# Kernel tuning notes

Hardware: AMD Instinct MI355X
Metric: run time of the kernel (lower is better)

Reference implementation:

```python
import jax, jax.numpy as jnp
import numpy as np

V, E, H, B, TE, TD = 32000, 256, 256, 32, 128, 64


def _gru_cell(x, h, Wi, Wh, bi, bh):
    # PyTorch GRU gate order: r, z, n
    gi = x @ Wi.T + bi            # [B, 3H]
    gh = h @ Wh.T + bh            # [B, 3H]
    i_r, i_z, i_n = jnp.split(gi, 3, axis=-1)
    h_r, h_z, h_n = jnp.split(gh, 3, axis=-1)
    r = jax.nn.sigmoid(i_r + h_r)
    z = jax.nn.sigmoid(i_z + h_z)
    n = jnp.tanh(i_n + r * h_n)
    return (1.0 - z) * n + z * h


def _run_gru(x_seq, h0, Wi, Wh, bi, bh, reverse=False):
    # x_seq: [B, T, D] -> outputs [B, T, H]
    xs = jnp.swapaxes(x_seq, 0, 1)  # [T, B, D]
    def step(h, x_t):
        h = _gru_cell(x_t, h, Wi, Wh, bi, bh)
        return h, h
    _, ys = jax.lax.scan(step, h0, xs, reverse=reverse)
    return jnp.swapaxes(ys, 0, 1)


def setup_inputs() -> dict:
    key = jax.random.key(0)
    ks = jax.random.split(key, 22)
    k = 1.0 / np.sqrt(H)
    u = lambda kk, shape, a: jax.random.uniform(kk, shape, jnp.float32, -a, a)
    return {
        'enc_in': jax.random.randint(ks[0], (B, TE), 0, V),
        'dec_in': jax.random.randint(ks[1], (B, TD), 0, V),
        'embed_W': u(ks[2], (V, E), 0.1),
        'Wi_f': u(ks[3], (3 * H, E), k), 'Wh_f': u(ks[4], (3 * H, H), k),
        'bi_f': u(ks[5], (3 * H,), k), 'bh_f': u(ks[6], (3 * H,), k),
        'Wi_b': u(ks[7], (3 * H, E), k), 'Wh_b': u(ks[8], (3 * H, H), k),
        'bi_b': u(ks[9], (3 * H,), k), 'bh_b': u(ks[10], (3 * H,), k),
        'Wi_d': u(ks[11], (3 * H, E + 2 * H), k), 'Wh_d': u(ks[12], (3 * H, H), k),
        'bi_d': u(ks[13], (3 * H,), k), 'bh_d': u(ks[14], (3 * H,), k),
        'W1_w': u(ks[15], (H, 2 * H), 1.0 / np.sqrt(2 * H)), 'W1_b': u(ks[16], (H,), 1.0 / np.sqrt(2 * H)),
        'W2_w': u(ks[17], (2 * H, H), k), 'W2_b': u(ks[18], (2 * H,), k),
        'lin_w': u(ks[19], (V, H), 0.1), 'lin_b': jnp.zeros((V,), jnp.float32),
    }


def reference(enc_in, dec_in, embed_W, Wi_f, Wh_f, bi_f, bh_f, Wi_b, Wh_b, bi_b, bh_b,
              Wi_d, Wh_d, bi_d, bh_d, W1_w, W1_b, W2_w, W2_b, lin_w, lin_b):
    # ---- encoder (bidirectional GRU, 1 layer) ----
    enc_emb = embed_W[enc_in]                                   # [B, TE, E]
    h0 = jnp.zeros((B, H), enc_emb.dtype)
    out_f = _run_gru(enc_emb, h0, Wi_f, Wh_f, bi_f, bh_f)       # [B, TE, H]
    out_b = _run_gru(enc_emb, h0, Wi_b, Wh_b, bi_b, bh_b, reverse=True)
    encoded = jnp.concatenate([out_f, out_b], axis=-1)          # [B, TE, 2H]

    # last valid state per example: encoded[i, sizes[i]-1]
    sizes = (enc_in > 0).sum(axis=1)                            # [B]
    last_states = encoded[jnp.arange(B), sizes - 1]             # [B, 2H]

    # ---- decoder with Luong attention (teacher forcing) ----
    dec_emb = embed_W[dec_in]                                   # [B, TD, E]
    h_init = last_states @ W1_w.T + W1_b                        # [B, H]
    ctx_init = jnp.zeros((B, 2 * H), enc_emb.dtype)

    def dec_step(carry, x_t):
        h, ctx = carry
        inp = jnp.concatenate([ctx, x_t], axis=-1)              # [B, E+2H]
        h = _gru_cell(inp, h, Wi_d, Wh_d, bi_d, bh_d)           # [B, H]
        comp = h @ W2_w.T + W2_b                                # [B, 2H]
        scores = jax.nn.softmax(jnp.einsum('bte,be->bt', encoded, comp), axis=-1)
        ctx = jnp.einsum('bt,bte->be', scores, encoded)          # [B, 2H]
        return (h, ctx), h

    _, outs = jax.lax.scan(dec_step, (h_init, ctx_init), jnp.swapaxes(dec_emb, 0, 1))
    outs = jnp.swapaxes(outs, 0, 1)                             # [B, TD, H]
    logits = outs @ lin_w.T + lin_b                             # [B, TD, V]
    return logits
```

## Files before the change

kernel.cpp:

```cpp
#include <hip/hip_runtime.h>
#include <hip/hip_bf16.h>

#define Vv 32000
#define Ee 256
#define Hh 256
#define Bb 32
#define TEe 128
#define TDd 64

typedef __attribute__((ext_vector_type(4))) float f32x4;
typedef __attribute__((ext_vector_type(8))) short short8;
typedef __attribute__((ext_vector_type(2))) unsigned int uint2v;
typedef __attribute__((ext_vector_type(4))) unsigned int uint4v;

static __device__ __forceinline__ unsigned short f2bf(float f){
  unsigned u = __float_as_uint(f);
  u += 0x7fffu + ((u >> 16) & 1u);
  return (unsigned short)(u >> 16);
}
static __device__ __forceinline__ unsigned pack2(float a, float b){
  return ((unsigned)f2bf(b) << 16) | (unsigned)f2bf(a);
}
static __device__ __forceinline__ float dot8(uint4v u, const float* hh){
  float s = 0.f;
  #pragma unroll
  for (int i = 0; i < 4; ++i){
    unsigned w = u[i];
    s = fmaf(__uint_as_float(w << 16),        hh[2*i],   s);
    s = fmaf(__uint_as_float(w & 0xffff0000u), hh[2*i+1], s);
  }
  return s;
}
static __device__ __forceinline__ float sigmoidf_(float x){
  return 1.f / (1.f + __expf(-x));
}

__global__ void k_sizes(const int* __restrict__ enc_in, int* __restrict__ sizes){
  int b = threadIdx.x;
  if (b < Bb){
    int c = 0;
    for (int t = 0; t < TEe; ++t) c += (enc_in[b*TEe + t] > 0);
    sizes[b] = c;
  }
}

__global__ void k_gather(const int* __restrict__ tok, const float* __restrict__ embW,
                         float* __restrict__ out, int rows){
  int i = blockIdx.x * 256 + threadIdx.x;
  int r = i >> 8, c = i & 255;
  if (r < rows) out[i] = embW[(size_t)tok[r]*Ee + c];
}

__global__ void k_extract_bf16(const float* __restrict__ src, unsigned short* __restrict__ dst,
                               int n){
  int i = blockIdx.x * 256 + threadIdx.x;
  if (i < n) dst[i] = f2bf(src[i]);
}

__global__ void k_chunkw(const float* __restrict__ src, unsigned short* __restrict__ dst, int rows){
  int idx = blockIdx.x * 256 + threadIdx.x;
  if (idx < rows * 256){
    int i = idx & 7, r = (idx >> 3) % rows, kb = idx / (rows * 8);
    dst[idx] = f2bf(src[(size_t)r*256 + kb*8 + i]);
  }
}

__global__ void k_projchunk(const float* __restrict__ in, unsigned short* __restrict__ out){
  int idx = blockIdx.x * 256 + threadIdx.x;
  int i = idx & 7;
  int t1 = idx >> 3;
  int n = t1 % 768;
  int t2 = t1 / 768;
  int kb = t2 & 15, b = t2 >> 4;
  out[idx] = f2bf(in[(size_t)(b*TEe + kb*8 + i)*768 + n]);
}

template<bool A_BF16, bool B_BF16, bool B_KMAJOR, bool OUT_BF16>
__global__ __launch_bounds__(256) void k_gemm(
  const void* __restrict__ Av, const void* __restrict__ Bv,
  const float* __restrict__ bias, void* __restrict__ Cv,
  int M, int N, int K, int lda, int ldb, int ldc)
{
  __shared__ unsigned short lA[128*40];
  __shared__ unsigned short lB[128*40];
  const int tid  = threadIdx.x;
  const int lane = tid & 63;
  const int w = tid >> 6, wr = w >> 1, wc = w & 1;
  const int m0 = blockIdx.y * 128, n0 = blockIdx.x * 128;
  f32x4 acc[4][4];
  #pragma unroll
  for (int i = 0; i < 4; ++i)
    #pragma unroll
    for (int j = 0; j < 4; ++j) acc[i][j] = (f32x4){0.f,0.f,0.f,0.f};

  for (int k0 = 0; k0 < K; k0 += 32){
    if (A_BF16){
      const unsigned short* A = (const unsigned short*)Av;
      #pragma unroll
      for (int it = 0; it < 2; ++it){
        int idx = tid + it*256; int r = idx >> 2, q = idx & 3;
        *(uint4v*)&lA[r*40 + q*8] = *(const uint4v*)(A + (size_t)(m0+r)*lda + k0 + q*8);
      }
    } else {
      const float* A = (const float*)Av;
      #pragma unroll
      for (int it = 0; it < 4; ++it){
        int idx = tid + it*256; int r = idx >> 3, q = idx & 7;
        f32x4 v = *(const f32x4*)(A + (size_t)(m0+r)*lda + k0 + q*4);
        uint2v pk; pk[0] = pack2(v[0], v[1]); pk[1] = pack2(v[2], v[3]);
        *(uint2v*)&lA[r*40 + q*4] = pk;
      }
    }
    if (B_KMAJOR){
      const float* Bp = (const float*)Bv;
      #pragma unroll
      for (int it = 0; it < 4; ++it){
        int idx = tid + it*256; int kk = idx >> 5, nq = idx & 31;
        f32x4 v = *(const f32x4*)(Bp + (size_t)(k0+kk)*ldb + n0 + nq*4);
        #pragma unroll
        for (int s2 = 0; s2 < 4; ++s2) lB[(nq*4+s2)*40 + kk] = f2bf(v[s2]);
      }
    } else if (B_BF16){
      const unsigned short* Bp = (const unsigned short*)Bv;
      #pragma unroll
      for (int it = 0; it < 2; ++it){
        int idx = tid + it*256; int r = idx >> 2, q = idx & 3;
        *(uint4v*)&lB[r*40 + q*8] = *(const uint4v*)(Bp + (size_t)(n0+r)*ldb + k0 + q*8);
      }
    } else {
      const float* Bp = (const float*)Bv;
      #pragma unroll
      for (int it = 0; it < 4; ++it){
        int idx = tid + it*256; int r = idx >> 3, q = idx & 7;
        f32x4 v = *(const f32x4*)(Bp + (size_t)(n0+r)*ldb + k0 + q*4);
        uint2v pk; pk[0] = pack2(v[0], v[1]); pk[1] = pack2(v[2], v[3]);
        *(uint2v*)&lB[r*40 + q*4] = pk;
      }
    }
    __syncthreads();
    short8 av[4], bv[4];
    #pragma unroll
    for (int i = 0; i < 4; ++i)
      av[i] = *(const short8*)&lA[(wr*64 + i*16 + (lane&15))*40 + (lane>>4)*8];
    #pragma unroll
    for (int j = 0; j < 4; ++j)
      bv[j] = *(const short8*)&lB[(wc*64 + j*16 + (lane&15))*40 + (lane>>4)*8];
    #pragma unroll
    for (int i = 0; i < 4; ++i)
      #pragma unroll
      for (int j = 0; j < 4; ++j)
        acc[i][j] = __builtin_amdgcn_mfma_f32_16x16x32_bf16(av[i], bv[j], acc[i][j], 0, 0, 0);
    __syncthreads();
  }
  #pragma unroll
  for (int i = 0; i < 4; ++i){
    #pragma unroll
    for (int j = 0; j < 4; ++j){
      int col = n0 + wc*64 + j*16 + (lane & 15);
      float bb = bias ? bias[col] : 0.f;
      #pragma unroll
      for (int r = 0; r < 4; ++r){
        int row = m0 + wr*64 + i*16 + (lane>>4)*4 + r;
        float v = acc[i][j][r] + bb;
        if (OUT_BF16) ((unsigned short*)Cv)[(size_t)row*ldc + col] = f2bf(v);
        else          ((float*)Cv)[(size_t)row*ldc + col] = v;
      }
    }
  }
}

__global__ __launch_bounds__(1024) void k_encoder(
  const unsigned short* __restrict__ Whf, const unsigned short* __restrict__ Whb,
  const float* __restrict__ bhf, const float* __restrict__ bhb,
  const float* __restrict__ gif, const float* __restrict__ gib,
  float* __restrict__ encoded)
{
  extern __shared__ char smem[];
  unsigned short* lw = (unsigned short*)smem;
  float* hA   = (float*)(smem + 131072);
  float* hB   = (float*)(smem + 132096);
  float* parA = (float*)(smem + 133120);
  float* parB = (float*)(smem + 137216);
  const int dir = blockIdx.x & 1, b = blockIdx.x >> 1;
  const unsigned short* Wh = dir ? Whb : Whf;
  const float* bh = dir ? bhb : bhf;
  const float* gi = dir ? gib : gif;
  const int T = threadIdx.x;
  const int rl = T & 255, q4 = T >> 8;
  const int rrh = T & 511, hf = T >> 9;
  const unsigned short* wsrc = Wh + (size_t)(hf*16)*6144 + (size_t)(256 + rrh)*8;
  uint4v wb[8];
  #pragma unroll
  for (int d = 0; d < 8; ++d) wb[d] = *(const uint4v*)(wsrc + (size_t)d*6144);
  for (int cc = T; cc < 256*32; cc += 1024){
    int r = cc >> 5, q = cc & 31;
    *(uint4v*)&lw[(r*32 + (q ^ (r & 31)))*8] = *(const uint4v*)(Wh + (size_t)q*6144 + r*8);
  }
  float bh0 = 0.f, bh1 = 0.f, bh2 = 0.f;
  if (T < 256){ bh0 = bh[T]; bh1 = bh[T+256]; bh2 = bh[T+512]; hA[T] = 0.f; }
  __syncthreads();
  const float* hc = hA; float* hn = hB;
  for (int s = 0; s < TEe; ++s){
    const int t = dir ? (TEe-1-s) : s;
    float aL = 0.f;
    #pragma unroll
    for (int i = 0; i < 8; ++i){
      const int ck = q4*8 + i;
      float hr[8];
      *(f32x4*)&hr[0] = *(const f32x4*)&hc[ck*8];
      *(f32x4*)&hr[4] = *(const f32x4*)&hc[ck*8+4];
      aL += dot8(*(const uint4v*)&lw[(rl*32 + (ck ^ (rl & 31)))*8], hr);
    }
    parA[q4*256 + rl] = aL;
    float aR = 0.f;
    const float* hh = hc + hf*128;
    #pragma unroll
    for (int q = 0; q < 16; ++q){
      float hr[8];
      *(f32x4*)&hr[0] = *(const f32x4*)&hh[q*8];
      *(f32x4*)&hr[4] = *(const f32x4*)&hh[q*8+4];
      aR += dot8(wb[q & 7], hr);
      wb[q & 7] = *(const uint4v*)(wsrc + (size_t)((q < 8) ? (q + 8) : (q - 8))*6144);
    }
    parB[hf*512 + rrh] = aR;
    __syncthreads();
    if (T < 256){
      const int j = T;
      const float* grow = gi + (size_t)(b*TEe + t)*768;
      const float A0 = parA[j] + parA[256+j] + parA[512+j] + parA[768+j] + bh0;
      const float A1 = parB[j] + parB[512+j] + bh1;
      const float A2 = parB[256+j] + parB[768+j] + bh2;
      const float r = sigmoidf_(grow[j] + A0);
      const float z = sigmoidf_(grow[j+256] + A1);
      const float n = tanhf(grow[j+512] + r*A2);
      const float hnew = (1.f - z)*n + z*hc[j];
      hn[j] = hnew;
      encoded[(size_t)(b*TEe + t)*512 + dir*256 + j] = hnew;
    }
    __syncthreads();
    const float* tmp = hc; hc = hn; hn = (float*)tmp;
  }
}

__global__ void k_encb2(const float* __restrict__ encoded, const float* __restrict__ W2b,
                        float* __restrict__ encb2){
  int r = blockIdx.x, l = threadIdx.x;
  const float* e = encoded + (size_t)r*512;
  float s = 0.f;
  for (int k = l; k < 512; k += 64) s += e[k]*W2b[k];
  for (int off = 32; off; off >>= 1) s += __shfl_down(s, off);
  if (l == 0) encb2[r] = s;
}

__global__ void k_hinit(const float* __restrict__ encoded, const int* __restrict__ sizes,
                        const float* __restrict__ W1w, const float* __restrict__ W1b,
                        float* __restrict__ h0){
  int b = blockIdx.x, o = threadIdx.x;
  int idx = sizes[b] - 1;
  idx = idx < 0 ? 0 : (idx > TEe-1 ? TEe-1 : idx);
  const float* ls = encoded + (size_t)(b*TEe + idx)*512;
  const float* wv = W1w + (size_t)o*512;
  float s = W1b[o];
  for (int k = 0; k < 512; k += 4){
    f32x4 a = *(const f32x4*)(ls + k);
    f32x4 w4 = *(const f32x4*)(wv + k);
    s = fmaf(a[0],w4[0], fmaf(a[1],w4[1], fmaf(a[2],w4[2], fmaf(a[3],w4[3], s))));
  }
  h0[b*256 + o] = s;
}

#define DLR 128
__global__ __launch_bounds__(512, 1) void k_decoder(
  const unsigned short* __restrict__ Whd, const float* __restrict__ bhd,
  const float* __restrict__ gidx,
  const unsigned short* __restrict__ encw2,
  const float* __restrict__ encb2,
  const unsigned short* __restrict__ projt,
  const float* __restrict__ h0,
  unsigned short* __restrict__ outs_bf)
{
  extern __shared__ char smem[];
  unsigned short* le = (unsigned short*)smem;
  unsigned short* lw = (unsigned short*)(smem + 65536);
  float* h    = (float*)(smem + 131072);
  float* parL = (float*)(smem + 132096);
  float* parS1= (float*)(smem + 134144);
  float* parS2= (float*)(smem + 136192);
  float* gcs  = (float*)(smem + 138240);
  float* cpar = (float*)(smem + 140288);
  float* p    = (float*)(smem + 142336);
  float* ebl  = (float*)(smem + 142848);
  const int b = blockIdx.x, T = threadIdx.x;
  const unsigned short* ptc = projt + (size_t)b*98304;
  const unsigned short* wsrcM = Whd + (size_t)(DLR + T)*8;
  const int trow = 640 + (T >> 2), tq = (T & 3)*8;
  const unsigned short* wsrcT = Whd + (size_t)trow*8;
  const unsigned short* csrcM = ptc + (size_t)T*8;
  const int crow = 512 + (T >> 1), cq = (T & 1)*8;
  const unsigned short* csrcT = ptc + (size_t)crow*8;
  uint4v wb[8], wb2[2], cb[4], cb2[2];
  #pragma unroll
  for (int d = 0; d < 8; ++d) wb[d] = *(const uint4v*)(wsrcM + (size_t)d*6144);
  wb2[0] = *(const uint4v*)(wsrcT + (size_t)tq*6144);
  wb2[1] = *(const uint4v*)(wsrcT + (size_t)(tq+1)*6144);
  #pragma unroll
  for (int d = 0; d < 4; ++d) cb[d] = *(const uint4v*)(csrcM + (size_t)d*6144);
  cb2[0] = *(const uint4v*)(csrcT + (size_t)cq*6144);
  cb2[1] = *(const uint4v*)(csrcT + (size_t)(cq+1)*6144);
  for (int cc = T; cc < 128*32; cc += 512){
    int r = cc >> 5, q = cc & 31;
    *(uint4v*)&le[(r*32 + (q ^ (r & 31)))*8] =
        *(const uint4v*)(encw2 + ((size_t)(b*TEe + r) << 8) + (q << 3));
  }
  for (int cc = T; cc < DLR*32; cc += 512){
    int r = cc >> 5, q = cc & 31;
    *(uint4v*)&lw[(r*32 + (q ^ (r & 31)))*8] =
        *(const uint4v*)(Whd + (size_t)q*6144 + r*8);
  }
  for (int i = T; i < 256; i += 512) h[i] = h0[b*256 + i];
  gcs[T] = 0.f; cpar[T] = 0.f;
  if (T < TEe) ebl[T] = encb2[b*TEe + T];
  float bh0 = 0.f, bh1 = 0.f, bh2 = 0.f;
  if (T < 256){ bh0 = bhd[T]; bh1 = bhd[T+256]; bh2 = bhd[T+512]; }
  __syncthreads();
  float g0 = 0.f, g1 = 0.f, g2 = 0.f;
  if (T < 256){
    const float* grow = gidx + (size_t)(b*TDd)*768;
    g0 = grow[T]; g1 = grow[T+256]; g2 = grow[T+512];
  }
  #define DOTS_BODY                                                            \
  {                                                                            \
    { const int rL2 = T >> 2, qb = (T & 3)*8;                                  \
      const unsigned short* lwr = lw + rL2*256;                                \
      float a = 0.f;                                                           \
      _Pragma("unroll")                                                        \
      for (int i = 0; i < 8; ++i){                                             \
        const int q = qb + i;                                                  \
        float hr[8];                                                           \
        *(f32x4*)&hr[0] = *(const f32x4*)&h[q*8];                              \
        *(f32x4*)&hr[4] = *(const f32x4*)&h[q*8+4];                            \
        a += dot8(*(const uint4v*)(lwr + ((q ^ (rL2 & 31)) << 3)), hr);        \
      }                                                                        \
      parL[(T & 3)*128 + rL2] = a;                                             \
    }                                                                          \
    { float a = 0.f;                                                           \
      _Pragma("unroll")                                                        \
      for (int q = 0; q < 32; ++q){                                            \
        float hr[8];                                                           \
        *(f32x4*)&hr[0] = *(const f32x4*)&h[q*8];                              \
        *(f32x4*)&hr[4] = *(const f32x4*)&h[q*8+4];                            \
        a += dot8(wb[q & 7], hr);                                              \
        wb[q & 7] = *(const uint4v*)(wsrcM + (size_t)((q < 24) ? (q + 8) : (q - 24))*6144); \
      }                                                                        \
      parS1[T] = a;                                                            \
    }                                                                          \
    { float a = 0.f;                                                           \
      _Pragma("unroll")                                                        \
      for (int i = 0; i < 8; ++i){                                             \
        const int q = tq + i;                                                  \
        float hr[8];                                                           \
        *(f32x4*)&hr[0] = *(const f32x4*)&h[q*8];                              \
        *(f32x4*)&hr[4] = *(const f32x4*)&h[q*8+4];                            \
        a += dot8(wb2[i & 1], hr);                                             \
        wb2[i & 1] = *(const uint4v*)(wsrcT + (size_t)(tq + ((i < 6) ? (i + 2) : (i - 6)))*6144); \
      }                                                                        \
      parS2[(T & 3)*128 + (T >> 2)] = a;                                       \
    }                                                                          \
  }
  DOTS_BODY
  __syncthreads();
  for (int t = 0; t < TDd; ++t){
    if (T < 256){
      const int j = T;
      float A0, A2;
      if (j < 128){
        A0 = parL[j] + parL[128+j] + parL[256+j] + parL[384+j];
        A2 = parS1[384+j];
      } else {
        A0 = parS1[j-128];
        A2 = parS2[j-128] + parS2[j] + parS2[j+128] + parS2[j+256];
      }
      const float A1 = parS1[128+j];
      const float gcr = gcs[j];
      const float gcz = gcs[256+j];
      const float gcn = cpar[j] + cpar[256+j];
      const float r = sigmoidf_(g0 + gcr + A0 + bh0);
      const float z = sigmoidf_(g1 + gcz + A1 + bh1);
      const float n = tanhf(g2 + gcn + r*(A2 + bh2));
      const float hnew = (1.f - z)*n + z*h[j];
      h[j] = hnew;
      outs_bf[(size_t)(b*TDd + t)*256 + j] = f2bf(hnew);
    }
    if (t + 1 == TDd) break;
    __syncthreads();
    if (T < 256){
      const float* grow = gidx + (size_t)(b*TDd + t + 1)*768;
      g0 = grow[T]; g1 = grow[T+256]; g2 = grow[T+512];
    }
    DOTS_BODY
    {
      const int pos = T >> 2, kq = (T & 3)*8;
      const unsigned short* er = le + pos*256;
      float s = 0.f;
      #pragma unroll
      for (int i = 0; i < 8; ++i){
        const int q = kq + i;
        float hr[8];
        *(f32x4*)&hr[0] = *(const f32x4*)&h[q*8];
        *(f32x4*)&hr[4] = *(const f32x4*)&h[q*8+4];
        s += dot8(*(const uint4v*)(er + ((q ^ (pos & 31)) << 3)), hr);
      }
      s += __shfl_xor(s, 1);
      s += __shfl_xor(s, 2);
      if ((T & 3) == 0) p[pos] = s + ebl[pos];
    }
    __syncthreads();
    if (T < 64){
      float m = fmaxf(p[T], p[T+64]);
      for (int off = 32; off; off >>= 1) m = fmaxf(m, __shfl_xor(m, off));
      float e0 = __expf(p[T] - m), e1 = __expf(p[T+64] - m);
      float ss = e0 + e1;
      for (int off = 32; off; off >>= 1) ss += __shfl_xor(ss, off);
      float inv = 1.f / ss;
      p[T] = e0*inv; p[T+64] = e1*inv;
    }
    __syncthreads();
    {
      float c = 0.f;
      #pragma unroll
      for (int q = 0; q < 16; ++q){
        float pr[8];
        *(f32x4*)&pr[0] = *(const f32x4*)&p[q*8];
        *(f32x4*)&pr[4] = *(const f32x4*)&p[q*8+4];
        c += dot8(cb[q & 3], pr);
        cb[q & 3] = *(const uint4v*)(csrcM + (size_t)((q < 12) ? (q + 4) : (q - 12))*6144);
      }
      gcs[T] = c;
      float c2 = 0.f;
      #pragma unroll
      for (int i = 0; i < 8; ++i){
        const int q = cq + i;
        float pr[8];
        *(f32x4*)&pr[0] = *(const f32x4*)&p[q*8];
        *(f32x4*)&pr[4] = *(const f32x4*)&p[q*8+4];
        c2 += dot8(cb2[i & 1], pr);
        cb2[i & 1] = *(const uint4v*)(csrcT + (size_t)(cq + ((i < 6) ? (i + 2) : (i - 6)))*6144);
      }
      cpar[(T & 1)*256 + (T >> 1)] = c2;
    }
    __syncthreads();
  }
  #undef DOTS_BODY
}

extern "C" void kernel_launch(void* const* d_in, const int* in_sizes, int n_in,
                              void* d_out, int out_size, void* d_ws, size_t ws_size,
                              hipStream_t stream)
{
  (void)in_sizes; (void)n_in; (void)out_size;
  const int*   enc_in = (const int*)d_in[0];
  const int*   dec_in = (const int*)d_in[1];
  const float* embW   = (const float*)d_in[2];
  const float* Wi_f   = (const float*)d_in[3];
  const float* Wh_f   = (const float*)d_in[4];
  const float* bi_f   = (const float*)d_in[5];
  const float* bh_f   = (const float*)d_in[6];
  const float* Wi_b   = (const float*)d_in[7];
  const float* Wh_b   = (const float*)d_in[8];
  const float* bi_b   = (const float*)d_in[9];
  const float* bh_b   = (const float*)d_in[10];
  const float* Wi_d   = (const float*)d_in[11];
  const float* Wh_d   = (const float*)d_in[12];
  const float* bi_d   = (const float*)d_in[13];
  const float* bh_d   = (const float*)d_in[14];
  const float* W1_w   = (const float*)d_in[15];
  const float* W1_b   = (const float*)d_in[16];
  const float* W2_w   = (const float*)d_in[17];
  const float* W2_b   = (const float*)d_in[18];
  const float* lin_w  = (const float*)d_in[19];
  const float* lin_b  = (const float*)d_in[20];

  char* scr = (char*)d_out;
  float* emb_enc = (float*)(scr + 0);
  float* emb_dec = (float*)(scr + 4194304);
  float* gi_f    = (float*)(scr + 6291456);
  float* gi_b    = (float*)(scr + 18874368);
  float* gi_dx   = (float*)(scr + 31457280);
  float* enc     = (float*)(scr + 37748736);
  float* projf   = (float*)(scr + 46137344);
  unsigned short* whf_bf = (unsigned short*)(scr + 58720256);
  unsigned short* whb_bf = (unsigned short*)(scr + 59113472);
  unsigned short* whd_bf = (unsigned short*)(scr + 59506688);
  unsigned short* encw2  = (unsigned short*)(scr + 59899904);
  unsigned short* projt  = (unsigned short*)(scr + 61997056);
  float* encb2 = (float*)(scr + 68288512);
  int*   sizes = (int*)(scr + 68304896);
  float* h0    = (float*)(scr + 68305024);

  unsigned short* outs_bf = (unsigned short*)d_ws;
  unsigned short* lin_bf  = (unsigned short*)((char*)d_ws + (1<<20));
  const bool big = ws_size >= (size_t)(1<<20) + 16384000u + 1024u;

  hipFuncSetAttribute((const void*)k_encoder, hipFuncAttributeMaxDynamicSharedMemorySize, 141312);
  hipFuncSetAttribute((const void*)k_decoder, hipFuncAttributeMaxDynamicSharedMemorySize, 143360);

  k_sizes<<<1, 32, 0, stream>>>(enc_in, sizes);
  k_gather<<<Bb*TEe, 256, 0, stream>>>(enc_in, embW, emb_enc, Bb*TEe);
  k_gather<<<Bb*TDd, 256, 0, stream>>>(dec_in, embW, emb_dec, Bb*TDd);
  k_chunkw<<<768, 256, 0, stream>>>(Wh_f, whf_bf, 768);
  k_chunkw<<<768, 256, 0, stream>>>(Wh_b, whb_bf, 768);
  k_chunkw<<<768, 256, 0, stream>>>(Wh_d, whd_bf, 768);
  if (big) k_extract_bf16<<<32000, 256, 0, stream>>>(lin_w, lin_bf, 32000*256);

  k_gemm<false,false,false,false><<<dim3(6,32), 256, 0, stream>>>(
      emb_enc, Wi_f, bi_f, gi_f, 4096, 768, 256, 256, 256, 768);
  k_gemm<false,false,false,false><<<dim3(6,32), 256, 0, stream>>>(
      emb_enc, Wi_b, bi_b, gi_b, 4096, 768, 256, 256, 256, 768);
  k_gemm<false,false,false,false><<<dim3(6,16), 256, 0, stream>>>(
      emb_dec, Wi_d + 512, bi_d, gi_dx, 2048, 768, 256, 256, 768, 768);

  k_encoder<<<64, 1024, 141312, stream>>>(whf_bf, whb_bf, bh_f, bh_b, gi_f, gi_b, enc);
  k_encb2<<<Bb*TEe, 64, 0, stream>>>(enc, W2_b, encb2);

  k_gemm<false,false,true,true><<<dim3(2,32), 256, 0, stream>>>(
      enc, W2_w, nullptr, encw2, 4096, 256, 512, 512, 256, 256);
  k_gemm<false,false,false,false><<<dim3(6,32), 256, 0, stream>>>(
      enc, Wi_d, nullptr, projf, 4096, 768, 512, 512, 768, 768);
  k_projchunk<<<(Bb*16*768*8)/256, 256, 0, stream>>>(projf, projt);
  k_hinit<<<Bb, 256, 0, stream>>>(enc, sizes, W1_w, W1_b, h0);

  k_decoder<<<Bb, 512, 143360, stream>>>(whd_bf, bh_d, gi_dx, encw2, encb2, projt, h0, outs_bf);

  if (big)
    k_gemm<true,true,false,false><<<dim3(250,16), 256, 0, stream>>>(
        outs_bf, lin_bf, lin_b, d_out, 2048, 32000, 256, 256, 256, 32000);
  else
    k_gemm<true,false,false,false><<<dim3(250,16), 256, 0, stream>>>(
        outs_bf, lin_w, lin_b, d_out, 2048, 32000, 256, 256, 256, 32000);
}
```

Baseline: 1.703 ms.

## Overlap lin_w bf16 conversion with encoder and feed bf16 operands to GEMMs

The separate lin_w fp32-to-bf16 conversion kernel is folded into the encoder launch as 128 extra blocks. These run alongside the 64 latency-bound recurrent blocks, so the large conversion can hide behind the sequential encoder. The input-projection, W2 and Wi_d GEMMs now take pre-converted bf16 weights and bf16 embeddings and encoder outputs, and the projection is written directly in bf16, which halves intermediate traffic. The extra blocks compete for memory bandwidth and CUs with the encoder, and the encoder now also writes a bf16 copy of its output.

```diff
diff --git a/kernel.cpp b/kernel.cpp
--- a/kernel.cpp
+++ b/kernel.cpp
@@ -45,16 +45,10 @@
 }
 
 __global__ void k_gather(const int* __restrict__ tok, const float* __restrict__ embW,
-                         float* __restrict__ out, int rows){
+                         unsigned short* __restrict__ out, int rows){
   int i = blockIdx.x * 256 + threadIdx.x;
   int r = i >> 8, c = i & 255;
-  if (r < rows) out[i] = embW[(size_t)tok[r]*Ee + c];
-}
-
-__global__ void k_extract_bf16(const float* __restrict__ src, unsigned short* __restrict__ dst,
-                               int n){
-  int i = blockIdx.x * 256 + threadIdx.x;
-  if (i < n) dst[i] = f2bf(src[i]);
+  if (r < rows) out[i] = f2bf(embW[(size_t)tok[r]*Ee + c]);
 }
 
 __global__ void k_chunkw(const float* __restrict__ src, unsigned short* __restrict__ dst, int rows){
@@ -65,14 +59,29 @@
   }
 }
 
-__global__ void k_projchunk(const float* __restrict__ in, unsigned short* __restrict__ out){
+__global__ void k_convert(const float* __restrict__ Wi_f, const float* __restrict__ Wi_b,
+                          const float* __restrict__ Wi_d, const float* __restrict__ W2_w,
+                          unsigned short* __restrict__ wif, unsigned short* __restrict__ wib,
+                          unsigned short* __restrict__ wid, unsigned short* __restrict__ w2t){
+  int idx = blockIdx.x * 256 + threadIdx.x;
+  if (idx < 196608)        wif[idx] = f2bf(Wi_f[idx]);
+  else if (idx < 393216)   wib[idx - 196608] = f2bf(Wi_b[idx - 196608]);
+  else if (idx < 983040)   wid[idx - 393216] = f2bf(Wi_d[idx - 393216]);
+  else if (idx < 1114112){
+    int l = idx - 983040;
+    int n = l >> 9, k = l & 511;
+    w2t[l] = f2bf(W2_w[k*256 + n]);
+  }
+}
+
+__global__ void k_projchunk(const unsigned short* __restrict__ in, unsigned short* __restrict__ out){
   int idx = blockIdx.x * 256 + threadIdx.x;
   int i = idx & 7;
   int t1 = idx >> 3;
   int n = t1 % 768;
   int t2 = t1 / 768;
   int kb = t2 & 15, b = t2 >> 4;
-  out[idx] = f2bf(in[(size_t)(b*TEe + kb*8 + i)*768 + n]);
+  out[idx] = in[(size_t)(b*TEe + kb*8 + i)*768 + n];
 }
 
 template<bool A_BF16, bool B_BF16, bool B_KMAJOR, bool OUT_BF16>
@@ -173,8 +182,17 @@
   const unsigned short* __restrict__ Whf, const unsigned short* __restrict__ Whb,
   const float* __restrict__ bhf, const float* __restrict__ bhb,
   const float* __restrict__ gif, const float* __restrict__ gib,
-  float* __restrict__ encoded)
+  float* __restrict__ encoded, unsigned short* __restrict__ encoded_bf,
+  const float* __restrict__ lin_w, unsigned short* __restrict__ lin_bf, int do_lin)
 {
+  if (blockIdx.x >= 64){
+    if (do_lin){
+      const int nlin = Vv*Hh;
+      for (int i = (blockIdx.x - 64)*1024 + threadIdx.x; i < nlin; i += 128*1024)
+        lin_bf[i] = f2bf(lin_w[i]);
+    }
+    return;
+  }
   extern __shared__ char smem[];
   unsigned short* lw = (unsigned short*)smem;
   float* hA   = (float*)(smem + 131072);
@@ -235,7 +253,9 @@
       const float n = tanhf(grow[j+512] + r*A2);
       const float hnew = (1.f - z)*n + z*hc[j];
       hn[j] = hnew;
-      encoded[(size_t)(b*TEe + t)*512 + dir*256 + j] = hnew;
+      const size_t off = (size_t)(b*TEe + t)*512 + dir*256 + j;
+      encoded[off] = hnew;
+      encoded_bf[off] = f2bf(hnew);
     }
     __syncthreads();
     const float* tmp = hc; hc = hn; hn = (float*)tmp;
@@ -330,12 +350,12 @@
   }
   #define DOTS_BODY                                                            \
   {                                                                            \
-    { const int rL2 = T >> 2, qb = (T & 3)*8;                                  \
+    { const int rL2 = T >> 2, qb2 = (T & 3)*8;                                 \
       const unsigned short* lwr = lw + rL2*256;                                \
       float a = 0.f;                                                           \
       _Pragma("unroll")                                                        \
       for (int i = 0; i < 8; ++i){                                             \
-        const int q = qb + i;                                                  \
+        const int q = qb2 + i;                                                 \
         float hr[8];                                                           \
         *(f32x4*)&hr[0] = *(const f32x4*)&h[q*8];                              \
         *(f32x4*)&hr[4] = *(const f32x4*)&h[q*8+4];                            \
@@ -481,21 +501,26 @@
   const float* lin_b  = (const float*)d_in[20];
 
   char* scr = (char*)d_out;
-  float* emb_enc = (float*)(scr + 0);
-  float* emb_dec = (float*)(scr + 4194304);
-  float* gi_f    = (float*)(scr + 6291456);
-  float* gi_b    = (float*)(scr + 18874368);
-  float* gi_dx   = (float*)(scr + 31457280);
-  float* enc     = (float*)(scr + 37748736);
-  float* projf   = (float*)(scr + 46137344);
-  unsigned short* whf_bf = (unsigned short*)(scr + 58720256);
-  unsigned short* whb_bf = (unsigned short*)(scr + 59113472);
-  unsigned short* whd_bf = (unsigned short*)(scr + 59506688);
-  unsigned short* encw2  = (unsigned short*)(scr + 59899904);
-  unsigned short* projt  = (unsigned short*)(scr + 61997056);
-  float* encb2 = (float*)(scr + 68288512);
-  int*   sizes = (int*)(scr + 68304896);
-  float* h0    = (float*)(scr + 68305024);
+  unsigned short* emb_enc = (unsigned short*)(scr + 0);
+  unsigned short* emb_dec = (unsigned short*)(scr + 2097152);
+  float* gi_f    = (float*)(scr + 3145728);
+  float* gi_b    = (float*)(scr + 15728640);
+  float* gi_dx   = (float*)(scr + 28311552);
+  float* enc     = (float*)(scr + 34603008);
+  unsigned short* enc_bf  = (unsigned short*)(scr + 42991616);
+  unsigned short* projf_bf= (unsigned short*)(scr + 47185920);
+  unsigned short* whf_bf = (unsigned short*)(scr + 53477376);
+  unsigned short* whb_bf = (unsigned short*)(scr + 53870592);
+  unsigned short* whd_bf = (unsigned short*)(scr + 54263808);
+  unsigned short* encw2  = (unsigned short*)(scr + 54657024);
+  unsigned short* projt  = (unsigned short*)(scr + 56754176);
+  unsigned short* wif_bf = (unsigned short*)(scr + 63045632);
+  unsigned short* wib_bf = (unsigned short*)(scr + 63438848);
+  unsigned short* wid_bf = (unsigned short*)(scr + 63832064);
+  unsigned short* w2t_bf = (unsigned short*)(scr + 65011712);
+  float* encb2 = (float*)(scr + 65273856);
+  int*   sizes = (int*)(scr + 65290240);
+  float* h0    = (float*)(scr + 65290368);
 
   unsigned short* outs_bf = (unsigned short*)d_ws;
   unsigned short* lin_bf  = (unsigned short*)((char*)d_ws + (1<<20));
@@ -510,23 +535,24 @@
   k_chunkw<<<768, 256, 0, stream>>>(Wh_f, whf_bf, 768);
   k_chunkw<<<768, 256, 0, stream>>>(Wh_b, whb_bf, 768);
   k_chunkw<<<768, 256, 0, stream>>>(Wh_d, whd_bf, 768);
-  if (big) k_extract_bf16<<<32000, 256, 0, stream>>>(lin_w, lin_bf, 32000*256);
-
-  k_gemm<false,false,false,false><<<dim3(6,32), 256, 0, stream>>>(
-      emb_enc, Wi_f, bi_f, gi_f, 4096, 768, 256, 256, 256, 768);
-  k_gemm<false,false,false,false><<<dim3(6,32), 256, 0, stream>>>(
-      emb_enc, Wi_b, bi_b, gi_b, 4096, 768, 256, 256, 256, 768);
-  k_gemm<false,false,false,false><<<dim3(6,16), 256, 0, stream>>>(
-      emb_dec, Wi_d + 512, bi_d, gi_dx, 2048, 768, 256, 256, 768, 768);
-
-  k_encoder<<<64, 1024, 141312, stream>>>(whf_bf, whb_bf, bh_f, bh_b, gi_f, gi_b, enc);
+  k_convert<<<4352, 256, 0, stream>>>(Wi_f, Wi_b, Wi_d, W2_w, wif_bf, wib_bf, wid_bf, w2t_bf);
+
+  k_gemm<true,true,false,false><<<dim3(6,32), 256, 0, stream>>>(
+      emb_enc, wif_bf, bi_f, gi_f, 4096, 768, 256, 256, 256, 768);
+  k_gemm<true,true,false,false><<<dim3(6,32), 256, 0, stream>>>(
+      emb_enc, wib_bf, bi_b, gi_b, 4096, 768, 256, 256, 256, 768);
+  k_gemm<true,true,false,false><<<dim3(6,16), 256, 0, stream>>>(
+      emb_dec, wid_bf + 512, bi_d, gi_dx, 2048, 768, 256, 256, 768, 768);
+
+  k_encoder<<<192, 1024, 141312, stream>>>(whf_bf, whb_bf, bh_f, bh_b, gi_f, gi_b,
+                                           enc, enc_bf, lin_w, lin_bf, big ? 1 : 0);
   k_encb2<<<Bb*TEe, 64, 0, stream>>>(enc, W2_b, encb2);
 
-  k_gemm<false,false,true,true><<<dim3(2,32), 256, 0, stream>>>(
-      enc, W2_w, nullptr, encw2, 4096, 256, 512, 512, 256, 256);
-  k_gemm<false,false,false,false><<<dim3(6,32), 256, 0, stream>>>(
-      enc, Wi_d, nullptr, projf, 4096, 768, 512, 512, 768, 768);
-  k_projchunk<<<(Bb*16*768*8)/256, 256, 0, stream>>>(projf, projt);
+  k_gemm<true,true,false,true><<<dim3(2,32), 256, 0, stream>>>(
+      enc_bf, w2t_bf, nullptr, encw2, 4096, 256, 512, 512, 512, 256);
+  k_gemm<true,true,false,true><<<dim3(6,32), 256, 0, stream>>>(
+      enc_bf, wid_bf, nullptr, projf_bf, 4096, 768, 512, 512, 768, 768);
+  k_projchunk<<<(Bb*16*768*8)/256, 256, 0, stream>>>(projf_bf, projt);
   k_hinit<<<Bb, 256, 0, stream>>>(enc, sizes, W1_w, W1_b, h0);
 
   k_decoder<<<Bb, 512, 143360, stream>>>(whd_bf, bh_d, gi_dx, encw2, encb2, projt, h0, outs_bf);
```

Result: faster. 1.650 ms (-3.1%).
